# Kernel tuning notes

Hardware: AMD Instinct MI355X
Metric: run time of the kernel (lower is better)

## Reference

```python
import jax, jax.numpy as jnp
import numpy as np
import math

DIM = 1024
HEADS = 16
B, N = 2, 2048

POLY = jnp.array([-0.037, 0.481, -2.3, 4.917, -1.791], dtype=jnp.float32)


def adaptive_temperature_softmax(logits):
    # logits: [b, h, n, n]
    original_probs = jax.nn.softmax(logits, axis=-1)
    entropy = jnp.sum(-original_probs * jnp.log(original_probs + 1e-9), axis=-1, keepdims=True)
    e2 = entropy * entropy
    poly_result = POLY[0] * e2 * e2 + POLY[1] * e2 * entropy + POLY[2] * e2 + POLY[3] * entropy + POLY[4]
    beta = jnp.where(entropy > 0.5, jnp.maximum(poly_result, 1.0), 1.0)
    return jax.nn.softmax(logits * beta, axis=-1)


def setup_inputs() -> dict:
    key = jax.random.key(0)
    ks = jax.random.split(key, 5)
    s = 1.0 / math.sqrt(DIM)
    return {
        "x": jax.random.normal(ks[0], (B, N, DIM), dtype=jnp.float32),
        "Wq": jax.random.normal(ks[1], (DIM, DIM), dtype=jnp.float32) * s,
        "Wk": jax.random.normal(ks[2], (DIM, DIM), dtype=jnp.float32) * s,
        "Wv": jax.random.normal(ks[3], (DIM, DIM), dtype=jnp.float32) * s,
        "Wo": jax.random.normal(ks[4], (DIM, DIM), dtype=jnp.float32) * s,
        "bo": jnp.zeros((DIM,), dtype=jnp.float32),
    }


def reference(x, Wq, Wk, Wv, Wo, bo):
    b, n, d = x.shape
    h = HEADS
    hd = d // h
    # torch nn.Linear: y = x @ W.T (+ bias)
    def proj(W):
        t = x @ W.T  # [b, n, d]
        return t.reshape(b, n, h, hd).transpose(0, 2, 1, 3)  # [b, h, n, hd]
    q, k, v = proj(Wq), proj(Wk), proj(Wv)
    sim = jnp.einsum('bhid,bhjd->bhij', q, k) / math.sqrt(hd)
    neg = -jnp.finfo(sim.dtype).max
    causal = jnp.triu(jnp.ones((n, n), dtype=bool), k=1)  # True above diagonal
    sim = jnp.where(causal, neg, sim)
    attn = adaptive_temperature_softmax(sim)
    out = jnp.einsum('bhij,bhjd->bhid', attn, v)
    out = out.transpose(0, 2, 1, 3).reshape(b, n, d)
    return out @ Wo.T + bo
```

## Files before the change

### kernel.cpp

```cpp
#include <hip/hip_runtime.h>
#include <math.h>

#define B_   2
#define N_   2048
#define D_   1024
#define H_   16
#define HD_  64
#define BH_  32
#define M_   4096

typedef __bf16 bf16x8 __attribute__((ext_vector_type(8)));
typedef float  f32x4  __attribute__((ext_vector_type(4)));

__device__ inline unsigned short f2b(float f) {
    unsigned u = __float_as_uint(f);
    u += 0x7FFFu + ((u >> 16) & 1u);
    return (unsigned short)(u >> 16);
}
__device__ inline unsigned short f2b_fast(float f) {
    return (unsigned short)((__float_as_uint(f) + 0x8000u) >> 16);
}

__global__ __launch_bounds__(256)
void cvt_all(const float* __restrict__ x,  const float* __restrict__ wq,
             const float* __restrict__ wk, const float* __restrict__ wv,
             const float* __restrict__ wo, ushort* __restrict__ dst)
{
    int i = blockIdx.x * 256 + threadIdx.x;
    if (i >= 2097152) return;
    int fi = i * 4;
    const float* s; int off;
    if (fi < 4194304) { s = x; off = fi; }
    else {
        int r = fi - 4194304;
        int wsel = r >> 20;
        off = r & 1048575;
        s = (wsel == 0) ? wq : (wsel == 1) ? wk : (wsel == 2) ? wv : wo;
    }
    float4 f = *(const float4*)(s + off);
    ushort4 o;
    o.x = f2b(f.x); o.y = f2b(f.y); o.z = f2b(f.z); o.w = f2b(f.w);
    *(ushort4*)(dst + fi) = o;
}

__global__ __launch_bounds__(256)
void gemm_qkv(const ushort* __restrict__ A,
              const ushort* __restrict__ W0, const ushort* __restrict__ W1,
              const ushort* __restrict__ W2,
              ushort* __restrict__ O0, ushort* __restrict__ O1,
              ushort* __restrict__ O2)
{
    const int z = blockIdx.z;
    const ushort* W = (z == 0) ? W0 : (z == 1) ? W1 : W2;

    __shared__ alignas(16) ushort As[128][40];
    __shared__ alignas(16) ushort Bs[128][40];

    const int t = threadIdx.x;
    const int lane = t & 63, w = t >> 6;
    const int quad = lane >> 4, l15 = lane & 15;
    const int wm = (w >> 1) * 64, wn = (w & 1) * 64;
    const int tileM = blockIdx.x * 128, tileN = blockIdx.y * 128;

    const int r0 = t >> 2, r1 = 64 + (t >> 2);
    const int cg = (t & 3) * 8;
    const ushort* GA0 = A + (size_t)(tileM + r0) * D_ + cg;
    const ushort* GA1 = A + (size_t)(tileM + r1) * D_ + cg;
    const ushort* GB0 = W + (size_t)(tileN + r0) * D_ + cg;
    const ushort* GB1 = W + (size_t)(tileN + r1) * D_ + cg;

    f32x4 acc[4][4];
#pragma unroll
    for (int mt = 0; mt < 4; ++mt)
#pragma unroll
        for (int nt = 0; nt < 4; ++nt) acc[mt][nt] = (f32x4){0.f, 0.f, 0.f, 0.f};

    uint4 pa0 = *(const uint4*)GA0, pa1 = *(const uint4*)GA1;
    uint4 pb0 = *(const uint4*)GB0, pb1 = *(const uint4*)GB1;

    for (int k0 = 0; k0 < D_; k0 += 32) {
        __syncthreads();
        *(uint4*)&As[r0][cg] = pa0;
        *(uint4*)&As[r1][cg] = pa1;
        *(uint4*)&Bs[r0][cg] = pb0;
        *(uint4*)&Bs[r1][cg] = pb1;
        __syncthreads();
        if (k0 + 32 < D_) {
            pa0 = *(const uint4*)(GA0 + k0 + 32);
            pa1 = *(const uint4*)(GA1 + k0 + 32);
            pb0 = *(const uint4*)(GB0 + k0 + 32);
            pb1 = *(const uint4*)(GB1 + k0 + 32);
        }

        bf16x8 af[4], bf[4];
#pragma unroll
        for (int mt = 0; mt < 4; ++mt) af[mt] = *(const bf16x8*)&As[wm + mt * 16 + l15][quad * 8];
#pragma unroll
        for (int nt = 0; nt < 4; ++nt) bf[nt] = *(const bf16x8*)&Bs[wn + nt * 16 + l15][quad * 8];
#pragma unroll
        for (int mt = 0; mt < 4; ++mt)
#pragma unroll
            for (int nt = 0; nt < 4; ++nt)
                acc[mt][nt] = __builtin_amdgcn_mfma_f32_16x16x32_bf16(af[mt], bf[nt], acc[mt][nt], 0, 0, 0);
    }

    ushort* O = (z == 0) ? O0 : (z == 1) ? O1 : O2;
    const float scl = (z == 0) ? 0.18033688f : 1.0f;
#pragma unroll
    for (int mt = 0; mt < 4; ++mt)
#pragma unroll
        for (int nt = 0; nt < 4; ++nt) {
            if (z == 2) {
                int rg0 = tileM + wm + mt * 16 + quad * 4;
                int cgc = tileN + wn + nt * 16 + l15;
                int b = rg0 >> 11, n0 = rg0 & (N_ - 1);
                int h = cgc >> 6, dd = cgc & 63;
                ushort4 o4;
                o4.x = f2b(acc[mt][nt][0]); o4.y = f2b(acc[mt][nt][1]);
                o4.z = f2b(acc[mt][nt][2]); o4.w = f2b(acc[mt][nt][3]);
                *(ushort4*)&O[((size_t)((b * H_ + h) * HD_ + dd)) * N_ + n0] = o4;
            } else {
#pragma unroll
                for (int r = 0; r < 4; ++r) {
                    int rg = tileM + wm + mt * 16 + quad * 4 + r;
                    int cgc = tileN + wn + nt * 16 + l15;
                    int b = rg >> 11, n = rg & (N_ - 1);
                    int h = cgc >> 6, dd = cgc & 63;
                    O[(((size_t)(b * H_ + h)) * N_ + n) * HD_ + dd] = f2b(acc[mt][nt][r] * scl);
                }
            }
        }
}

__global__ __launch_bounds__(256)
void gemm_fin(const ushort* __restrict__ A, const ushort* __restrict__ W,
              const float* __restrict__ bias, float* __restrict__ Of)
{
    __shared__ alignas(16) ushort As[128][40];
    __shared__ alignas(16) ushort Bs[64][40];

    const int t = threadIdx.x;
    const int lane = t & 63, w = t >> 6;
    const int quad = lane >> 4, l15 = lane & 15;
    const int wm = (w >> 1) * 64, wn = (w & 1) * 32;
    const int tileM = blockIdx.x * 128, tileN = blockIdx.y * 64;

    const int r0 = t >> 2, r1 = 64 + (t >> 2);
    const int cg = (t & 3) * 8;
    const ushort* GA0 = A + (size_t)(tileM + r0) * D_ + cg;
    const ushort* GA1 = A + (size_t)(tileM + r1) * D_ + cg;
    const ushort* GB0 = W + (size_t)(tileN + r0) * D_ + cg;

    f32x4 acc[4][2];
#pragma unroll
    for (int mt = 0; mt < 4; ++mt)
#pragma unroll
        for (int nt = 0; nt < 2; ++nt) acc[mt][nt] = (f32x4){0.f, 0.f, 0.f, 0.f};

    uint4 pa0 = *(const uint4*)GA0, pa1 = *(const uint4*)GA1;
    uint4 pb0 = *(const uint4*)GB0;

    for (int k0 = 0; k0 < D_; k0 += 32) {
        __syncthreads();
        *(uint4*)&As[r0][cg] = pa0;
        *(uint4*)&As[r1][cg] = pa1;
        *(uint4*)&Bs[r0 & 63][cg] = pb0;
        __syncthreads();
        if (k0 + 32 < D_) {
            pa0 = *(const uint4*)(GA0 + k0 + 32);
            pa1 = *(const uint4*)(GA1 + k0 + 32);
            pb0 = *(const uint4*)(GB0 + k0 + 32);
        }

        bf16x8 af[4], bf[2];
#pragma unroll
        for (int mt = 0; mt < 4; ++mt) af[mt] = *(const bf16x8*)&As[wm + mt * 16 + l15][quad * 8];
#pragma unroll
        for (int nt = 0; nt < 2; ++nt) bf[nt] = *(const bf16x8*)&Bs[wn + nt * 16 + l15][quad * 8];
#pragma unroll
        for (int mt = 0; mt < 4; ++mt)
#pragma unroll
            for (int nt = 0; nt < 2; ++nt)
                acc[mt][nt] = __builtin_amdgcn_mfma_f32_16x16x32_bf16(af[mt], bf[nt], acc[mt][nt], 0, 0, 0);
    }

#pragma unroll
    for (int mt = 0; mt < 4; ++mt)
#pragma unroll
        for (int nt = 0; nt < 2; ++nt)
#pragma unroll
            for (int r = 0; r < 4; ++r) {
                int rg = tileM + wm + mt * 16 + quad * 4 + r;
                int cgc = tileN + wn + nt * 16 + l15;
                Of[(size_t)rg * D_ + cgc] = acc[mt][nt][r] + bias[cgc];
            }
}

__global__ __launch_bounds__(256)
void attn_mfma(const ushort* __restrict__ Q, const ushort* __restrict__ K,
               const ushort* __restrict__ VT, ushort* __restrict__ AO)
{
    const int bid = blockIdx.x;
    const int p  = bid >> 5;
    const int bh = bid & 31;
    const size_t kvbase = (size_t)bh * N_ * HD_;

    __shared__ alignas(16) ushort Ks[64][72];
    __shared__ alignas(16) ushort Vt[64][72];
    __shared__ alignas(16) ushort Ps[4][4][296];

    const int t = threadIdx.x;
    const int lane = t & 63, w = t >> 6;
    const int quad = lane >> 4, l15 = lane & 15;
    const float SH2 = 11.5416913f;
    const float LN2 = 0.69314718f;

    const int skey = t >> 3;
    const int skc  = (t & 7) * 8;
    const ushort* KS0 = K  + kvbase + (size_t)skey * HD_ + skc;
    const ushort* KS1 = KS0 + 32 * HD_;
    const ushort* VS0 = VT + kvbase + (size_t)skey * N_ + skc;
    const ushort* VS1 = VS0 + 32 * N_;

    const int qrow = w * 16 + quad * 4;
    const int b = bh >> 4, h = bh & 15;

    for (int item = 0; item < 2; ++item) {
        const int qt = item ? p : (31 - p);

        bf16x8 aq0, aq1;
        {
            const size_t qr = kvbase + (size_t)(qt * 64 + w * 16 + l15) * HD_;
            aq0 = *(const bf16x8*)&Q[qr + quad * 8];
            aq1 = *(const bf16x8*)&Q[qr + 32 + quad * 8];
        }

        float ez[4] = {0.f, 0.f, 0.f, 0.f};
        float sz[4] = {0.f, 0.f, 0.f, 0.f};

        uint4 pk0 = *(const uint4*)KS0;
        uint4 pk1 = *(const uint4*)KS1;
        for (int kb = 0; kb <= qt; ++kb) {
            __syncthreads();
            *(uint4*)&Ks[skey][skc]      = pk0;
            *(uint4*)&Ks[32 + skey][skc] = pk1;
            __syncthreads();
            if (kb < qt) {
                pk0 = *(const uint4*)(KS0 + (size_t)(kb + 1) * (64 * HD_));
                pk1 = *(const uint4*)(KS1 + (size_t)(kb + 1) * (64 * HD_));
            }
            if (kb < qt) {
#pragma unroll
                for (int nt = 0; nt < 4; ++nt) {
                    f32x4 sv = (f32x4){0.f, 0.f, 0.f, 0.f};
                    sv = __builtin_amdgcn_mfma_f32_16x16x32_bf16(aq0, *(const bf16x8*)&Ks[nt * 16 + l15][quad * 8], sv, 0, 0, 0);
                    sv = __builtin_amdgcn_mfma_f32_16x16x32_bf16(aq1, *(const bf16x8*)&Ks[nt * 16 + l15][32 + quad * 8], sv, 0, 0, 0);
#pragma unroll
                    for (int r = 0; r < 4; ++r) {
                        float sh = sv[r] - SH2;
                        float e = __builtin_amdgcn_exp2f(sh);
                        ez[r] += e;
                        sz[r] = fmaf(e, sh, sz[r]);
                    }
                }
            } else {
#pragma unroll
                for (int nt = 0; nt < 4; ++nt) {
                    f32x4 sv = (f32x4){0.f, 0.f, 0.f, 0.f};
                    sv = __builtin_amdgcn_mfma_f32_16x16x32_bf16(aq0, *(const bf16x8*)&Ks[nt * 16 + l15][quad * 8], sv, 0, 0, 0);
                    sv = __builtin_amdgcn_mfma_f32_16x16x32_bf16(aq1, *(const bf16x8*)&Ks[nt * 16 + l15][32 + quad * 8], sv, 0, 0, 0);
                    const int kcol = nt * 16 + l15;
#pragma unroll
                    for (int r = 0; r < 4; ++r) {
                        float sh = sv[r] - SH2;
                        float e = (kcol <= qrow + r) ? __builtin_amdgcn_exp2f(sh) : 0.f;
                        ez[r] += e;
                        sz[r] = fmaf(e, sh, sz[r]);
                    }
                }
            }
        }
#pragma unroll
        for (int r = 0; r < 4; ++r) {
#pragma unroll
            for (int off = 1; off < 16; off <<= 1) {
                ez[r] += __shfl_xor(ez[r], off);
                sz[r] += __shfl_xor(sz[r], off);
            }
        }

        float nbs[4], bl[4];
#pragma unroll
        for (int r = 0; r < 4; ++r) {
            float Z = ez[r];
            float Hh = LN2 * (__builtin_amdgcn_logf(Z) - sz[r] / Z);
            float bb = 1.f;
            if (Hh > 0.5f) {
                float e2 = Hh * Hh;
                float pp = -0.037f * e2 * e2 + 0.481f * e2 * Hh - 2.3f * e2 + 4.917f * Hh - 1.791f;
                bb = fmaxf(pp, 1.f);
            }
            bl[r] = bb;
            nbs[r] = -bb * SH2;
        }

        f32x4 ov[4];
#pragma unroll
        for (int nt = 0; nt < 4; ++nt) ov[nt] = (f32x4){0.f, 0.f, 0.f, 0.f};
        float zp[4] = {0.f, 0.f, 0.f, 0.f};

        pk0 = *(const uint4*)KS0;
        pk1 = *(const uint4*)KS1;
        uint4 pv0 = *(const uint4*)VS0;
        uint4 pv1 = *(const uint4*)VS1;
        for (int kb = 0; kb <= qt; ++kb) {
            __syncthreads();
            *(uint4*)&Ks[skey][skc]      = pk0;
            *(uint4*)&Ks[32 + skey][skc] = pk1;
            *(uint4*)&Vt[skey][skc]      = pv0;
            *(uint4*)&Vt[32 + skey][skc] = pv1;
            __syncthreads();
            if (kb < qt) {
                pk0 = *(const uint4*)(KS0 + (size_t)(kb + 1) * (64 * HD_));
                pk1 = *(const uint4*)(KS1 + (size_t)(kb + 1) * (64 * HD_));
                pv0 = *(const uint4*)(VS0 + (kb + 1) * 64);
                pv1 = *(const uint4*)(VS1 + (kb + 1) * 64);
            }
            const bool diag = (kb == qt);

            float wv[4][4];
#pragma unroll
            for (int nt = 0; nt < 4; ++nt) {
                f32x4 sv = (f32x4){0.f, 0.f, 0.f, 0.f};
                sv = __builtin_amdgcn_mfma_f32_16x16x32_bf16(aq0, *(const bf16x8*)&Ks[nt * 16 + l15][quad * 8], sv, 0, 0, 0);
                sv = __builtin_amdgcn_mfma_f32_16x16x32_bf16(aq1, *(const bf16x8*)&Ks[nt * 16 + l15][32 + quad * 8], sv, 0, 0, 0);
                const int kcol = nt * 16 + l15;
#pragma unroll
                for (int r = 0; r < 4; ++r) {
                    float e = __builtin_amdgcn_exp2f(fmaf(bl[r], sv[r], nbs[r]));
                    wv[nt][r] = (!diag || (kcol <= qrow + r)) ? e : 0.f;
                }
            }
#pragma unroll
            for (int nt = 0; nt < 4; ++nt)
#pragma unroll
                for (int r = 0; r < 4; ++r)
                    Ps[w][quad][r * 72 + nt * 16 + l15] = f2b_fast(wv[nt][r]);
#pragma unroll
            for (int r = 0; r < 4; ++r)
                zp[r] += (wv[0][r] + wv[1][r]) + (wv[2][r] + wv[3][r]);

            bf16x8 pa0 = *(const bf16x8*)&Ps[w][l15 >> 2][(l15 & 3) * 72 + quad * 8];
            bf16x8 pa1 = *(const bf16x8*)&Ps[w][l15 >> 2][(l15 & 3) * 72 + 32 + quad * 8];
#pragma unroll
            for (int nt = 0; nt < 4; ++nt) {
                ov[nt] = __builtin_amdgcn_mfma_f32_16x16x32_bf16(pa0, *(const bf16x8*)&Vt[nt * 16 + l15][quad * 8], ov[nt], 0, 0, 0);
                ov[nt] = __builtin_amdgcn_mfma_f32_16x16x32_bf16(pa1, *(const bf16x8*)&Vt[nt * 16 + l15][32 + quad * 8], ov[nt], 0, 0, 0);
            }
        }
#pragma unroll
        for (int r = 0; r < 4; ++r)
#pragma unroll
            for (int off = 1; off < 16; off <<= 1) zp[r] += __shfl_xor(zp[r], off);

#pragma unroll
        for (int r = 0; r < 4; ++r) {
            int qg = qt * 64 + w * 16 + quad * 4 + r;
            float inv = 1.f / zp[r];
            size_t rowoff = ((size_t)(b * N_ + qg)) * D_ + h * HD_;
#pragma unroll
            for (int nt = 0; nt < 4; ++nt)
                AO[rowoff + nt * 16 + l15] = f2b(ov[nt][r] * inv);
        }
    }
}

extern "C" void kernel_launch(void* const* d_in, const int* in_sizes, int n_in,
                              void* d_out, int out_size, void* d_ws, size_t ws_size,
                              hipStream_t stream)
{
    const float* x  = (const float*)d_in[0];
    const float* Wq = (const float*)d_in[1];
    const float* Wk = (const float*)d_in[2];
    const float* Wv = (const float*)d_in[3];
    const float* Wo = (const float*)d_in[4];
    const float* bo = (const float*)d_in[5];
    float* out = (float*)d_out;

    ushort* ws  = (ushort*)d_ws;
    ushort* xb  = ws;
    ushort* wqb = ws + 4194304;
    ushort* wkb = ws + 5242880;
    ushort* wvb = ws + 6291456;
    ushort* wob = ws + 7340032;
    ushort* Qb  = ws + 8388608;
    ushort* Kb  = ws + 12582912;
    ushort* Vtb = ws + 16777216;
    ushort* aob = ws + 20971520;

    cvt_all<<<8192, 256, 0, stream>>>(x, Wq, Wk, Wv, Wo, xb);

    gemm_qkv<<<dim3(32, 8, 3), 256, 0, stream>>>(
        xb, wqb, wkb, wvb, Qb, Kb, Vtb);

    attn_mfma<<<dim3(512), 256, 0, stream>>>(Qb, Kb, Vtb, aob);

    gemm_fin<<<dim3(32, 16), 256, 0, stream>>>(aob, wob, bo, out);
}
```

Before: 207.1 us.

## Give each attention block one query tile and stage K/V in 128-key chunks

The attention kernel previously paired a long and a short query tile per block (512 blocks). Now each of 1024 blocks handles a single query tile, ordered longest-first, and K/V are staged in 128-key chunks so there are half as many barrier rounds. This gives more parallelism and fewer syncs, in exchange for more shared memory per block (possibly lower occupancy), less even per-block work, and a partly runtime-bounded loop on the diagonal chunk.

```diff
diff --git a/kernel.cpp b/kernel.cpp
--- a/kernel.cpp
+++ b/kernel.cpp
@@ -201,12 +201,12 @@
                const ushort* __restrict__ VT, ushort* __restrict__ AO)
 {
     const int bid = blockIdx.x;
-    const int p  = bid >> 5;
+    const int qt = 31 - (bid >> 5);
     const int bh = bid & 31;
     const size_t kvbase = (size_t)bh * N_ * HD_;
 
-    __shared__ alignas(16) ushort Ks[64][72];
-    __shared__ alignas(16) ushort Vt[64][72];
+    __shared__ alignas(16) ushort Ks[128][72];
+    __shared__ alignas(16) ushort Vs[64][136];
     __shared__ alignas(16) ushort Ps[4][4][296];
 
     const int t = threadIdx.x;
@@ -217,123 +217,146 @@
 
     const int skey = t >> 3;
     const int skc  = (t & 7) * 8;
-    const ushort* KS0 = K  + kvbase + (size_t)skey * HD_ + skc;
-    const ushort* KS1 = KS0 + 32 * HD_;
-    const ushort* VS0 = VT + kvbase + (size_t)skey * N_ + skc;
-    const ushort* VS1 = VS0 + 32 * N_;
+    const ushort* KS = K + kvbase + (size_t)skey * HD_ + skc;
+    const int vhd = t >> 4;
+    const int vkc = (t & 15) * 8;
+    const ushort* VS = VT + kvbase + (size_t)vhd * N_ + vkc;
 
     const int qrow = w * 16 + quad * 4;
+    const int qglob = qt * 64 + qrow;
     const int b = bh >> 4, h = bh & 15;
-
-    for (int item = 0; item < 2; ++item) {
-        const int qt = item ? p : (31 - p);
-
-        bf16x8 aq0, aq1;
-        {
-            const size_t qr = kvbase + (size_t)(qt * 64 + w * 16 + l15) * HD_;
-            aq0 = *(const bf16x8*)&Q[qr + quad * 8];
-            aq1 = *(const bf16x8*)&Q[qr + 32 + quad * 8];
-        }
-
-        float ez[4] = {0.f, 0.f, 0.f, 0.f};
-        float sz[4] = {0.f, 0.f, 0.f, 0.f};
-
-        uint4 pk0 = *(const uint4*)KS0;
-        uint4 pk1 = *(const uint4*)KS1;
-        for (int kb = 0; kb <= qt; ++kb) {
-            __syncthreads();
-            *(uint4*)&Ks[skey][skc]      = pk0;
-            *(uint4*)&Ks[32 + skey][skc] = pk1;
-            __syncthreads();
-            if (kb < qt) {
-                pk0 = *(const uint4*)(KS0 + (size_t)(kb + 1) * (64 * HD_));
-                pk1 = *(const uint4*)(KS1 + (size_t)(kb + 1) * (64 * HD_));
-            }
-            if (kb < qt) {
-#pragma unroll
-                for (int nt = 0; nt < 4; ++nt) {
-                    f32x4 sv = (f32x4){0.f, 0.f, 0.f, 0.f};
-                    sv = __builtin_amdgcn_mfma_f32_16x16x32_bf16(aq0, *(const bf16x8*)&Ks[nt * 16 + l15][quad * 8], sv, 0, 0, 0);
-                    sv = __builtin_amdgcn_mfma_f32_16x16x32_bf16(aq1, *(const bf16x8*)&Ks[nt * 16 + l15][32 + quad * 8], sv, 0, 0, 0);
-#pragma unroll
-                    for (int r = 0; r < 4; ++r) {
-                        float sh = sv[r] - SH2;
-                        float e = __builtin_amdgcn_exp2f(sh);
-                        ez[r] += e;
-                        sz[r] = fmaf(e, sh, sz[r]);
-                    }
-                }
-            } else {
-#pragma unroll
-                for (int nt = 0; nt < 4; ++nt) {
-                    f32x4 sv = (f32x4){0.f, 0.f, 0.f, 0.f};
-                    sv = __builtin_amdgcn_mfma_f32_16x16x32_bf16(aq0, *(const bf16x8*)&Ks[nt * 16 + l15][quad * 8], sv, 0, 0, 0);
-                    sv = __builtin_amdgcn_mfma_f32_16x16x32_bf16(aq1, *(const bf16x8*)&Ks[nt * 16 + l15][32 + quad * 8], sv, 0, 0, 0);
-                    const int kcol = nt * 16 + l15;
-#pragma unroll
-                    for (int r = 0; r < 4; ++r) {
-                        float sh = sv[r] - SH2;
-                        float e = (kcol <= qrow + r) ? __builtin_amdgcn_exp2f(sh) : 0.f;
-                        ez[r] += e;
-                        sz[r] = fmaf(e, sh, sz[r]);
-                    }
-                }
-            }
-        }
-#pragma unroll
-        for (int r = 0; r < 4; ++r) {
-#pragma unroll
-            for (int off = 1; off < 16; off <<= 1) {
-                ez[r] += __shfl_xor(ez[r], off);
-                sz[r] += __shfl_xor(sz[r], off);
-            }
-        }
-
-        float nbs[4], bl[4];
-#pragma unroll
-        for (int r = 0; r < 4; ++r) {
-            float Z = ez[r];
-            float Hh = LN2 * (__builtin_amdgcn_logf(Z) - sz[r] / Z);
-            float bb = 1.f;
-            if (Hh > 0.5f) {
-                float e2 = Hh * Hh;
-                float pp = -0.037f * e2 * e2 + 0.481f * e2 * Hh - 2.3f * e2 + 4.917f * Hh - 1.791f;
-                bb = fmaxf(pp, 1.f);
-            }
-            bl[r] = bb;
-            nbs[r] = -bb * SH2;
-        }
-
-        f32x4 ov[4];
-#pragma unroll
-        for (int nt = 0; nt < 4; ++nt) ov[nt] = (f32x4){0.f, 0.f, 0.f, 0.f};
-        float zp[4] = {0.f, 0.f, 0.f, 0.f};
-
-        pk0 = *(const uint4*)KS0;
-        pk1 = *(const uint4*)KS1;
-        uint4 pv0 = *(const uint4*)VS0;
-        uint4 pv1 = *(const uint4*)VS1;
-        for (int kb = 0; kb <= qt; ++kb) {
-            __syncthreads();
-            *(uint4*)&Ks[skey][skc]      = pk0;
-            *(uint4*)&Ks[32 + skey][skc] = pk1;
-            *(uint4*)&Vt[skey][skc]      = pv0;
-            *(uint4*)&Vt[32 + skey][skc] = pv1;
-            __syncthreads();
-            if (kb < qt) {
-                pk0 = *(const uint4*)(KS0 + (size_t)(kb + 1) * (64 * HD_));
-                pk1 = *(const uint4*)(KS1 + (size_t)(kb + 1) * (64 * HD_));
-                pv0 = *(const uint4*)(VS0 + (kb + 1) * 64);
-                pv1 = *(const uint4*)(VS1 + (kb + 1) * 64);
-            }
-            const bool diag = (kb == qt);
-
-            float wv[4][4];
-#pragma unroll
-            for (int nt = 0; nt < 4; ++nt) {
+    const int nCh = (qt + 2) >> 1;
+
+    bf16x8 aq0, aq1;
+    {
+        const size_t qr = kvbase + (size_t)(qt * 64 + w * 16 + l15) * HD_;
+        aq0 = *(const bf16x8*)&Q[qr + quad * 8];
+        aq1 = *(const bf16x8*)&Q[qr + 32 + quad * 8];
+    }
+
+    float ez[4] = {0.f, 0.f, 0.f, 0.f};
+    float sz[4] = {0.f, 0.f, 0.f, 0.f};
+
+    uint4 k0 = *(const uint4*)KS;
+    uint4 k1 = *(const uint4*)(KS + 32 * HD_);
+    uint4 k2 = *(const uint4*)(KS + 64 * HD_);
+    uint4 k3 = *(const uint4*)(KS + 96 * HD_);
+    for (int c = 0; c < nCh; ++c) {
+        __syncthreads();
+        *(uint4*)&Ks[skey][skc]      = k0;
+        *(uint4*)&Ks[32 + skey][skc] = k1;
+        *(uint4*)&Ks[64 + skey][skc] = k2;
+        *(uint4*)&Ks[96 + skey][skc] = k3;
+        __syncthreads();
+        if (c + 1 < nCh) {
+            const ushort* nb = KS + (size_t)(c + 1) * (128 * HD_);
+            k0 = *(const uint4*)nb;
+            k1 = *(const uint4*)(nb + 32 * HD_);
+            k2 = *(const uint4*)(nb + 64 * HD_);
+            k3 = *(const uint4*)(nb + 96 * HD_);
+        }
+        if (c + 1 < nCh) {
+#pragma unroll
+            for (int nt = 0; nt < 8; ++nt) {
                 f32x4 sv = (f32x4){0.f, 0.f, 0.f, 0.f};
                 sv = __builtin_amdgcn_mfma_f32_16x16x32_bf16(aq0, *(const bf16x8*)&Ks[nt * 16 + l15][quad * 8], sv, 0, 0, 0);
                 sv = __builtin_amdgcn_mfma_f32_16x16x32_bf16(aq1, *(const bf16x8*)&Ks[nt * 16 + l15][32 + quad * 8], sv, 0, 0, 0);
+#pragma unroll
+                for (int r = 0; r < 4; ++r) {
+                    float sh = sv[r] - SH2;
+                    float e = __builtin_amdgcn_exp2f(sh);
+                    ez[r] += e;
+                    sz[r] = fmaf(e, sh, sz[r]);
+                }
+            }
+        } else {
+            const int tiles = (((qt + 1) * 64) - c * 128) >> 4;
+            const int kb0 = c * 128;
+            for (int nt = 0; nt < tiles; ++nt) {
+                f32x4 sv = (f32x4){0.f, 0.f, 0.f, 0.f};
+                sv = __builtin_amdgcn_mfma_f32_16x16x32_bf16(aq0, *(const bf16x8*)&Ks[nt * 16 + l15][quad * 8], sv, 0, 0, 0);
+                sv = __builtin_amdgcn_mfma_f32_16x16x32_bf16(aq1, *(const bf16x8*)&Ks[nt * 16 + l15][32 + quad * 8], sv, 0, 0, 0);
+                const int kcol = kb0 + nt * 16 + l15;
+#pragma unroll
+                for (int r = 0; r < 4; ++r) {
+                    float sh = sv[r] - SH2;
+                    float e = (kcol <= qglob + r) ? __builtin_amdgcn_exp2f(sh) : 0.f;
+                    ez[r] += e;
+                    sz[r] = fmaf(e, sh, sz[r]);
+                }
+            }
+        }
+    }
+#pragma unroll
+    for (int r = 0; r < 4; ++r) {
+#pragma unroll
+        for (int off = 1; off < 16; off <<= 1) {
+            ez[r] += __shfl_xor(ez[r], off);
+            sz[r] += __shfl_xor(sz[r], off);
+        }
+    }
+
+    float nbs[4], bl[4];
+#pragma unroll
+    for (int r = 0; r < 4; ++r) {
+        float Z = ez[r];
+        float Hh = LN2 * (__builtin_amdgcn_logf(Z) - sz[r] / Z);
+        float bb = 1.f;
+        if (Hh > 0.5f) {
+            float e2 = Hh * Hh;
+            float pp = -0.037f * e2 * e2 + 0.481f * e2 * Hh - 2.3f * e2 + 4.917f * Hh - 1.791f;
+            bb = fmaxf(pp, 1.f);
+        }
+        bl[r] = bb;
+        nbs[r] = -bb * SH2;
+    }
+
+    f32x4 ov[4];
+#pragma unroll
+    for (int nt = 0; nt < 4; ++nt) ov[nt] = (f32x4){0.f, 0.f, 0.f, 0.f};
+    float zp[4] = {0.f, 0.f, 0.f, 0.f};
+
+    k0 = *(const uint4*)KS;
+    k1 = *(const uint4*)(KS + 32 * HD_);
+    k2 = *(const uint4*)(KS + 64 * HD_);
+    k3 = *(const uint4*)(KS + 96 * HD_);
+    uint4 v0 = *(const uint4*)VS;
+    uint4 v1 = *(const uint4*)(VS + 16 * N_);
+    uint4 v2 = *(const uint4*)(VS + 32 * N_);
+    uint4 v3 = *(const uint4*)(VS + 48 * N_);
+    for (int c = 0; c < nCh; ++c) {
+        __syncthreads();
+        *(uint4*)&Ks[skey][skc]      = k0;
+        *(uint4*)&Ks[32 + skey][skc] = k1;
+        *(uint4*)&Ks[64 + skey][skc] = k2;
+        *(uint4*)&Ks[96 + skey][skc] = k3;
+        *(uint4*)&Vs[vhd][vkc]       = v0;
+        *(uint4*)&Vs[16 + vhd][vkc]  = v1;
+        *(uint4*)&Vs[32 + vhd][vkc]  = v2;
+        *(uint4*)&Vs[48 + vhd][vkc]  = v3;
+        __syncthreads();
+        if (c + 1 < nCh) {
+            const ushort* nk = KS + (size_t)(c + 1) * (128 * HD_);
+            k0 = *(const uint4*)nk;
+            k1 = *(const uint4*)(nk + 32 * HD_);
+            k2 = *(const uint4*)(nk + 64 * HD_);
+            k3 = *(const uint4*)(nk + 96 * HD_);
+            const ushort* nv = VS + (c + 1) * 128;
+            v0 = *(const uint4*)nv;
+            v1 = *(const uint4*)(nv + 16 * N_);
+            v2 = *(const uint4*)(nv + 32 * N_);
+            v3 = *(const uint4*)(nv + 48 * N_);
+        }
+        const int halves = min(2, (qt + 1) - c * 2);
+        for (int hh = 0; hh < halves; ++hh) {
+            const bool diag = (c * 2 + hh == qt);
+
+            float wv[4][4];
+#pragma unroll
+            for (int nt = 0; nt < 4; ++nt) {
+                f32x4 sv = (f32x4){0.f, 0.f, 0.f, 0.f};
+                sv = __builtin_amdgcn_mfma_f32_16x16x32_bf16(aq0, *(const bf16x8*)&Ks[hh * 64 + nt * 16 + l15][quad * 8], sv, 0, 0, 0);
+                sv = __builtin_amdgcn_mfma_f32_16x16x32_bf16(aq1, *(const bf16x8*)&Ks[hh * 64 + nt * 16 + l15][32 + quad * 8], sv, 0, 0, 0);
                 const int kcol = nt * 16 + l15;
 #pragma unroll
                 for (int r = 0; r < 4; ++r) {
@@ -354,24 +377,24 @@
             bf16x8 pa1 = *(const bf16x8*)&Ps[w][l15 >> 2][(l15 & 3) * 72 + 32 + quad * 8];
 #pragma unroll
             for (int nt = 0; nt < 4; ++nt) {
-                ov[nt] = __builtin_amdgcn_mfma_f32_16x16x32_bf16(pa0, *(const bf16x8*)&Vt[nt * 16 + l15][quad * 8], ov[nt], 0, 0, 0);
-                ov[nt] = __builtin_amdgcn_mfma_f32_16x16x32_bf16(pa1, *(const bf16x8*)&Vt[nt * 16 + l15][32 + quad * 8], ov[nt], 0, 0, 0);
-            }
-        }
-#pragma unroll
-        for (int r = 0; r < 4; ++r)
-#pragma unroll
-            for (int off = 1; off < 16; off <<= 1) zp[r] += __shfl_xor(zp[r], off);
-
-#pragma unroll
-        for (int r = 0; r < 4; ++r) {
-            int qg = qt * 64 + w * 16 + quad * 4 + r;
-            float inv = 1.f / zp[r];
-            size_t rowoff = ((size_t)(b * N_ + qg)) * D_ + h * HD_;
-#pragma unroll
-            for (int nt = 0; nt < 4; ++nt)
-                AO[rowoff + nt * 16 + l15] = f2b(ov[nt][r] * inv);
-        }
+                ov[nt] = __builtin_amdgcn_mfma_f32_16x16x32_bf16(pa0, *(const bf16x8*)&Vs[nt * 16 + l15][hh * 64 + quad * 8], ov[nt], 0, 0, 0);
+                ov[nt] = __builtin_amdgcn_mfma_f32_16x16x32_bf16(pa1, *(const bf16x8*)&Vs[nt * 16 + l15][hh * 64 + 32 + quad * 8], ov[nt], 0, 0, 0);
+            }
+        }
+    }
+#pragma unroll
+    for (int r = 0; r < 4; ++r)
+#pragma unroll
+        for (int off = 1; off < 16; off <<= 1) zp[r] += __shfl_xor(zp[r], off);
+
+#pragma unroll
+    for (int r = 0; r < 4; ++r) {
+        int qg = qt * 64 + w * 16 + quad * 4 + r;
+        float inv = 1.f / zp[r];
+        size_t rowoff = ((size_t)(b * N_ + qg)) * D_ + h * HD_;
+#pragma unroll
+        for (int nt = 0; nt < 4; ++nt)
+            AO[rowoff + nt * 16 + l15] = f2b(ov[nt][r] * inv);
     }
 }
 
@@ -403,7 +426,7 @@
     gemm_qkv<<<dim3(32, 8, 3), 256, 0, stream>>>(
         xb, wqb, wkb, wvb, Qb, Kb, Vtb);
 
-    attn_mfma<<<dim3(512), 256, 0, stream>>>(Qb, Kb, Vtb, aob);
+    attn_mfma<<<dim3(1024), 256, 0, stream>>>(Qb, Kb, Vtb, aob);
 
     gemm_fin<<<dim3(32, 16), 256, 0, stream>>>(aob, wob, bo, out);
 }
```

After: 202.2 us. 2.4% less time.
